# Performance work log

Hardware: AMD Instinct MI355X
Metric: run time of the kernel (lower is better)

Reference implementation:

```python
import jax, jax.numpy as jnp
import numpy as np

N_EMBED = 1024
HEAD_SIZE = 64
BLOCK_SIZE = 2048

def setup_inputs() -> dict:
    key = jax.random.key(0)
    kx, kq, kk, kv = jax.random.split(key, 4)
    scale = N_EMBED ** -0.5
    x = jax.random.normal(kx, (8, 2048, N_EMBED), dtype=jnp.float32)
    # nn.Linear weights stored as [out, in]; we keep [in, out] for x @ W
    Wq = jax.random.normal(kq, (N_EMBED, HEAD_SIZE), dtype=jnp.float32) * scale
    Wk = jax.random.normal(kk, (N_EMBED, HEAD_SIZE), dtype=jnp.float32) * scale
    Wv = jax.random.normal(kv, (N_EMBED, HEAD_SIZE), dtype=jnp.float32) * scale
    return {"x": x, "Wq": Wq, "Wk": Wk, "Wv": Wv}

def reference(x, Wq, Wk, Wv):
    B, T, C = x.shape
    q = x @ Wq  # [B,T,H]
    k = x @ Wk
    v = x @ Wv
    # NOTE: original scales by C**-0.5 (n_embed), not head_size**-0.5
    wei = jnp.einsum('bth,bsh->bts', q, k) * (C ** -0.5)  # [B,T,T]
    causal = jnp.tril(jnp.ones((T, T), dtype=bool))
    wei = jnp.where(causal, wei, -jnp.inf)
    wei = jax.nn.softmax(wei, axis=-1)
    out = jnp.einsum('bts,bsh->bth', wei, v)  # [B,T,H]
    return out
```

## Files before the change

### kernel.cpp

```cpp
#include <hip/hip_runtime.h>

#define B_ 8
#define T_ 2048
#define C_ 1024
#define H_ 64

typedef __attribute__((ext_vector_type(8))) short short8;
typedef __attribute__((ext_vector_type(4))) float floatx4;
typedef __attribute__((ext_vector_type(4))) int intx4;

static __device__ __forceinline__ unsigned short f2bf(float f) {
  unsigned int u = __builtin_bit_cast(unsigned int, f);
  u += 0x7FFFu + ((u >> 16) & 1u);
  return (unsigned short)(u >> 16);
}
static __device__ __forceinline__ float bf2f(unsigned short u) {
  return __builtin_bit_cast(float, ((unsigned int)u) << 16);
}
static __device__ __forceinline__ unsigned int fbits(float f) {
  return __builtin_bit_cast(unsigned int, f);
}

typedef const __attribute__((address_space(1))) unsigned int* gp1_t;
typedef __attribute__((address_space(3))) unsigned int* lp3_t;
static __device__ __forceinline__ void gl_lds16(const void* g, void* l) {
  __builtin_amdgcn_global_load_lds((gp1_t)g, (lp3_t)l, 16, 0, 0);
}

__global__ __launch_bounds__(256) void conv_w(const float* __restrict__ wq,
    const float* __restrict__ wk, const float* __restrict__ wv,
    unsigned short* __restrict__ wf) {
  int c = blockIdx.x * 256 + threadIdx.x;
  int lane = c & 63;
  int t = c >> 6;
  int ng = t % 12;
  int kk = t / 12;
  int k0 = kk * 32 + (lane >> 4) * 8;
  int n = ng * 16 + (lane & 15);
  const float* src;
  int col;
  float scale = 1.0f;
  if (n < 64)       { src = wq; col = n;       scale = 0.03125f * 1.44269504088896340736f; }
  else if (n < 128) { src = wk; col = n - 64;  }
  else              { src = wv; col = n - 128; }
  unsigned short o[8];
#pragma unroll
  for (int j = 0; j < 8; ++j) o[j] = f2bf(src[(size_t)(k0 + j) * H_ + col] * scale);
  *(uint4*)&wf[(size_t)c * 8] = *(const uint4*)o;
}

__global__ __launch_bounds__(256, 4) void qkv_proj(
    const float* __restrict__ x, const unsigned short* __restrict__ wf,
    unsigned short* __restrict__ qo, unsigned short* __restrict__ kf,
    unsigned short* __restrict__ vf) {
  __shared__ float XL[2][4096];
  int tid = threadIdx.x;
  int wave = tid >> 6, lane = tid & 63;
  int lane4 = lane & 15, quad = lane >> 4;
  int m0 = blockIdx.x * 32;
  int ph0 = blockIdx.x & 7;

  auto stage_ph = [&](int phr, int buf) {
#pragma unroll
    for (int j = 0; j < 4; ++j) {
      int c = (wave * 4 + j) * 64 + lane;
      int r = c >> 5, pc = c & 31;
      int cl = (pc & ~7) | ((pc ^ (r & 7)) & 7);
      gl_lds16(&x[(size_t)(m0 + r) * C_ + phr * 128 + cl * 4], &XL[buf][c * 4]);
    }
  };

  floatx4 acc[2][3];
#pragma unroll
  for (int mt = 0; mt < 2; ++mt)
#pragma unroll
    for (int nt = 0; nt < 3; ++nt) acc[mt][nt] = (floatx4)0.0f;

  stage_ph(ph0, 0);
  __syncthreads();

  for (int ph = 0; ph < 8; ++ph) {
    int buf = ph & 1;
    if (ph < 7) stage_ph((ph + 1 + ph0) & 7, buf ^ 1);
    int phr = (ph + ph0) & 7;
#pragma unroll
    for (int sl = 0; sl < 4; ++sl) {
      int s = phr * 4 + sl;
      short8 b[3];
#pragma unroll
      for (int nt = 0; nt < 3; ++nt)
        b[nt] = *(const short8*)&wf[(size_t)(s * 12 + wave * 3 + nt) * 512 + lane * 8];
      short8 a[2];
#pragma unroll
      for (int mt = 0; mt < 2; ++mt) {
        int r = mt * 16 + lane4;
        int c0 = sl * 8 + quad * 2;
        int pc0 = (c0 & ~7) | ((c0 ^ (r & 7)) & 7);
        int pc1 = ((c0 + 1) & ~7) | (((c0 + 1) ^ (r & 7)) & 7);
        float4 f0 = *(const float4*)&XL[buf][r * 128 + pc0 * 4];
        float4 f1 = *(const float4*)&XL[buf][r * 128 + pc1 * 4];
        intx4 pk;
        pk[0] = (int)__builtin_amdgcn_perm(fbits(f0.y), fbits(f0.x), 0x07060302u);
        pk[1] = (int)__builtin_amdgcn_perm(fbits(f0.w), fbits(f0.z), 0x07060302u);
        pk[2] = (int)__builtin_amdgcn_perm(fbits(f1.y), fbits(f1.x), 0x07060302u);
        pk[3] = (int)__builtin_amdgcn_perm(fbits(f1.w), fbits(f1.z), 0x07060302u);
        a[mt] = __builtin_bit_cast(short8, pk);
      }
#pragma unroll
      for (int mt = 0; mt < 2; ++mt)
#pragma unroll
        for (int nt = 0; nt < 3; ++nt)
          acc[mt][nt] = __builtin_amdgcn_mfma_f32_16x16x32_bf16(a[mt], b[nt], acc[mt][nt], 0, 0, 0);
    }
    __syncthreads();
  }

  unsigned short* VTB = (unsigned short*)&XL[0][0];
  unsigned short* KB  = VTB + 5120;
#pragma unroll
  for (int mt = 0; mt < 2; ++mt)
#pragma unroll
    for (int nt = 0; nt < 3; ++nt) {
      int n = wave * 48 + nt * 16 + lane4;
#pragma unroll
      for (int rr = 0; rr < 4; ++rr) {
        unsigned short val = f2bf(acc[mt][nt][rr]);
        int lrow = mt * 16 + quad * 4 + rr;
        if (n < 64)       qo[(size_t)(m0 + lrow) * H_ + n] = val;
        else if (n < 128) KB[lrow * 72 + (n - 64)] = val;
        else              VTB[(n - 128) * 40 + lrow] = val;
      }
    }
  __syncthreads();
  {
    int bb = m0 >> 11, t0 = m0 & 2047;
    int st = t0 >> 6, off = t0 & 63;
    int ks = tid >> 7, ctl = (tid >> 6) & 1, ln = tid & 63;
    int ct = (off >> 4) + ctl;
    int tl = ctl * 16 + (ln & 15);
    int h0 = ks * 32 + (ln >> 4) * 8;
    uint4 kd = *(const uint4*)&KB[tl * 72 + h0];
    *(uint4*)&kf[((size_t)((bb * 32 + st) * 2 + ks) * 4 + ct) * 512 + ln * 8] = kd;
    int nt = tid >> 6, l4 = tid & 15, qs = (tid >> 4) & 3;
    int ksv = off >> 5;
    uint2 vlo = *(const uint2*)&VTB[(nt * 16 + l4) * 40 + qs * 4];
    uint2 vhi = *(const uint2*)&VTB[(nt * 16 + l4) * 40 + 16 + qs * 4];
    uint4 vd = make_uint4(vlo.x, vlo.y, vhi.x, vhi.y);
    *(uint4*)&vf[((size_t)((bb * 32 + st) * 2 + ksv) * 4 + nt) * 512 + (tid & 63) * 8] = vd;
  }
}

__global__ __launch_bounds__(512, 4) void attn(
    const unsigned short* __restrict__ qi, const unsigned short* __restrict__ Kf,
    const unsigned short* __restrict__ Vf, unsigned short* __restrict__ Op,
    float* __restrict__ lsum) {
  __shared__ unsigned short KV[3][8192];

  int tid = threadIdx.x;
  int wave = tid >> 6, lane = tid & 63;
  int lane4 = lane & 15, quad = lane >> 4;
  int split = blockIdx.z;
  int qt = (split < 2) ? (15 - (int)blockIdx.x) : (int)blockIdx.x;
  int b = blockIdx.y;
  int qb = qt * 128;
  int base = b * T_;

  int ntile = 2 * qt + 2;
  int sBeg = (split * ntile) >> 2;
  int sEnd = ((split + 1) * ntile) >> 2;
  int last = sEnd - 1;

  short8 aq[2];
#pragma unroll
  for (int ks = 0; ks < 2; ++ks)
    aq[ks] = *(const short8*)&qi[(size_t)(base + qb + wave * 16 + lane4) * H_ + ks * 32 + quad * 8];

  float lsumv = 0.0f;
  floatx4 o[4];
#pragma unroll
  for (int nt = 0; nt < 4; ++nt) o[nt] = (floatx4)0.0f;

  auto stage = [&](int st, int bf) {
    size_t tb = (size_t)(b * 32 + st) * 4096;
    gl_lds16(&Kf[tb + (size_t)tid * 8], &KV[bf][tid * 8]);
    gl_lds16(&Vf[tb + (size_t)tid * 8], &KV[bf][4096 + tid * 8]);
  };

  if (sBeg < sEnd) {
    stage(sBeg, 0);
    {
      int s1 = sBeg + 1 <= last ? sBeg + 1 : last;
      stage(s1, 1);
    }

    for (int it = 0; it < sEnd - sBeg; ++it) {
      int st = sBeg + it;
      int buf = it % 3;

      asm volatile("s_waitcnt vmcnt(2)" ::: "memory");
      __builtin_amdgcn_sched_barrier(0);
      __builtin_amdgcn_s_barrier();

      {
        int s2 = st + 2 <= last ? st + 2 : last;
        stage(s2, (it + 2) % 3);
      }

      floatx4 sacc[4];
#pragma unroll
      for (int ct = 0; ct < 4; ++ct) sacc[ct] = (floatx4)0.0f;
      __builtin_amdgcn_s_setprio(1);
#pragma unroll
      for (int ks = 0; ks < 2; ++ks)
#pragma unroll
        for (int ct = 0; ct < 4; ++ct) {
          short8 bk = *(const short8*)&KV[buf][(ks * 4 + ct) * 512 + lane * 8];
          sacc[ct] = __builtin_amdgcn_mfma_f32_16x16x32_bf16(bk, aq[ks], sacc[ct], 0, 0, 0);
        }
      __builtin_amdgcn_s_setprio(0);

      if (st >= 2 * qt) {
        int qrow = qb + wave * 16 + lane4;
#pragma unroll
        for (int ct = 0; ct < 4; ++ct)
#pragma unroll
          for (int r = 0; r < 4; ++r) {
            int scol = st * 64 + ct * 16 + quad * 4 + r;
            if (scol > qrow) sacc[ct][r] = -3.0e38f;
          }
      }

      unsigned int pk[4][2];
#pragma unroll
      for (int ct = 0; ct < 4; ++ct) {
        float p0 = exp2f(sacc[ct][0] - 8.0f);
        float p1 = exp2f(sacc[ct][1] - 8.0f);
        float p2 = exp2f(sacc[ct][2] - 8.0f);
        float p3 = exp2f(sacc[ct][3] - 8.0f);
        lsumv += (p0 + p1) + (p2 + p3);
        pk[ct][0] = __builtin_amdgcn_perm(fbits(p1), fbits(p0), 0x07060302u);
        pk[ct][1] = __builtin_amdgcn_perm(fbits(p3), fbits(p2), 0x07060302u);
      }

      __builtin_amdgcn_s_setprio(1);
#pragma unroll
      for (int ks = 0; ks < 2; ++ks) {
        intx4 pai;
        pai[0] = (int)pk[2 * ks][0];
        pai[1] = (int)pk[2 * ks][1];
        pai[2] = (int)pk[2 * ks + 1][0];
        pai[3] = (int)pk[2 * ks + 1][1];
        short8 pa = __builtin_bit_cast(short8, pai);
#pragma unroll
        for (int nt = 0; nt < 4; ++nt) {
          short8 bv = *(const short8*)&KV[buf][4096 + (ks * 4 + nt) * 512 + lane * 8];
          o[nt] = __builtin_amdgcn_mfma_f32_16x16x32_bf16(pa, bv, o[nt], 0, 0, 0);
        }
      }
      __builtin_amdgcn_s_setprio(0);
    }
  }

  lsumv += __shfl_xor(lsumv, 16);
  lsumv += __shfl_xor(lsumv, 32);

  size_t pbase = (((size_t)split * 8 + b) * 16 + qt) * 128;
#pragma unroll
  for (int r = 0; r < 4; ++r) {
    int row = wave * 16 + quad * 4 + r;
#pragma unroll
    for (int nt = 0; nt < 4; ++nt)
      Op[(pbase + row) * 64 + nt * 16 + lane4] = f2bf(o[nt][r]);
  }
  if (quad == 0) lsum[pbase + wave * 16 + lane4] = lsumv;
}

__global__ __launch_bounds__(256) void merge_splits(
    const unsigned short* __restrict__ Op, const float* __restrict__ lsum,
    float* __restrict__ out) {
  int idx = blockIdx.x * 256 + threadIdx.x;
  int row = idx >> 4;
  int h4 = (idx & 15) * 4;
  int b = row >> 11, t = row & 2047;
  int qt = t >> 7, r = t & 127;
  float O0 = 0.f, O1 = 0.f, O2 = 0.f, O3 = 0.f, l = 0.f;
#pragma unroll
  for (int s = 0; s < 4; ++s) {
    size_t p = (((size_t)s * 8 + b) * 16 + qt) * 128 + r;
    l += lsum[p];
    ushort4 ov = *(const ushort4*)&Op[p * 64 + h4];
    O0 += bf2f(ov.x); O1 += bf2f(ov.y); O2 += bf2f(ov.z); O3 += bf2f(ov.w);
  }
  float inv = 1.0f / l;
  float4 res = make_float4(O0 * inv, O1 * inv, O2 * inv, O3 * inv);
  *(float4*)&out[(size_t)row * H_ + h4] = res;
}

extern "C" void kernel_launch(void* const* d_in, const int* in_sizes, int n_in,
                              void* d_out, int out_size, void* d_ws, size_t ws_size,
                              hipStream_t stream) {
  const float* x  = (const float*)d_in[0];
  const float* wq = (const float*)d_in[1];
  const float* wk = (const float*)d_in[2];
  const float* wv = (const float*)d_in[3];
  float* out = (float*)d_out;

  char* ws = (char*)d_ws;
  unsigned short* wf = (unsigned short*)ws;
  unsigned short* qb = (unsigned short*)(ws + 393216);
  unsigned short* kf = (unsigned short*)(ws + 2490368);
  unsigned short* vf = (unsigned short*)(ws + 4587520);
  unsigned short* Op = (unsigned short*)(ws + 6684672);
  float*          ls = (float*)(ws + 15073280);

  conv_w<<<96, 256, 0, stream>>>(wq, wk, wv, wf);
  qkv_proj<<<512, 256, 0, stream>>>(x, wf, qb, kf, vf);
  attn<<<dim3(16, 8, 4), 512, 0, stream>>>(qb, kf, vf, Op, ls);
  merge_splits<<<1024, 256, 0, stream>>>(Op, ls, out);
}
```

Before: 121.6 us.

## Process two 16-row query subtiles per wave in attention kernel

The attention block shrinks from 8 to 4 waves, and each wave now handles 32 query rows (two 16-row subtiles) instead of 16. Each K and V fragment read from LDS then feeds two MFMAs, halving LDS traffic per FLOP. Staging loads double per thread and the wait count is adjusted to match. The trade-off is higher register pressure and fewer waves per block to hide latency, with launch bounds set to 256 threads and 2 blocks per CU.

```diff
diff --git a/kernel.cpp b/kernel.cpp
--- a/kernel.cpp
+++ b/kernel.cpp
@@ -150,7 +150,7 @@
   }
 }
 
-__global__ __launch_bounds__(512, 4) void attn(
+__global__ __launch_bounds__(256, 2) void attn(
     const unsigned short* __restrict__ qi, const unsigned short* __restrict__ Kf,
     const unsigned short* __restrict__ Vf, unsigned short* __restrict__ Op,
     float* __restrict__ lsum) {
@@ -170,20 +170,26 @@
   int sEnd = ((split + 1) * ntile) >> 2;
   int last = sEnd - 1;
 
-  short8 aq[2];
-#pragma unroll
-  for (int ks = 0; ks < 2; ++ks)
-    aq[ks] = *(const short8*)&qi[(size_t)(base + qb + wave * 16 + lane4) * H_ + ks * 32 + quad * 8];
-
-  float lsumv = 0.0f;
-  floatx4 o[4];
-#pragma unroll
-  for (int nt = 0; nt < 4; ++nt) o[nt] = (floatx4)0.0f;
+  short8 aq[2][2];
+#pragma unroll
+  for (int sp = 0; sp < 2; ++sp)
+#pragma unroll
+    for (int ks = 0; ks < 2; ++ks)
+      aq[sp][ks] = *(const short8*)&qi[(size_t)(base + qb + wave * 32 + sp * 16 + lane4) * H_ + ks * 32 + quad * 8];
+
+  float lsumv0 = 0.0f, lsumv1 = 0.0f;
+  floatx4 o[2][4];
+#pragma unroll
+  for (int sp = 0; sp < 2; ++sp)
+#pragma unroll
+    for (int nt = 0; nt < 4; ++nt) o[sp][nt] = (floatx4)0.0f;
 
   auto stage = [&](int st, int bf) {
     size_t tb = (size_t)(b * 32 + st) * 4096;
     gl_lds16(&Kf[tb + (size_t)tid * 8], &KV[bf][tid * 8]);
+    gl_lds16(&Kf[tb + (size_t)(tid + 256) * 8], &KV[bf][(tid + 256) * 8]);
     gl_lds16(&Vf[tb + (size_t)tid * 8], &KV[bf][4096 + tid * 8]);
+    gl_lds16(&Vf[tb + (size_t)(tid + 256) * 8], &KV[bf][4096 + (tid + 256) * 8]);
   };
 
   if (sBeg < sEnd) {
@@ -197,7 +203,7 @@
       int st = sBeg + it;
       int buf = it % 3;
 
-      asm volatile("s_waitcnt vmcnt(2)" ::: "memory");
+      asm volatile("s_waitcnt vmcnt(4)" ::: "memory");
       __builtin_amdgcn_sched_barrier(0);
       __builtin_amdgcn_s_barrier();
 
@@ -206,73 +212,95 @@
         stage(s2, (it + 2) % 3);
       }
 
-      floatx4 sacc[4];
-#pragma unroll
-      for (int ct = 0; ct < 4; ++ct) sacc[ct] = (floatx4)0.0f;
+      floatx4 sacc[2][4];
+#pragma unroll
+      for (int sp = 0; sp < 2; ++sp)
+#pragma unroll
+        for (int ct = 0; ct < 4; ++ct) sacc[sp][ct] = (floatx4)0.0f;
       __builtin_amdgcn_s_setprio(1);
 #pragma unroll
       for (int ks = 0; ks < 2; ++ks)
 #pragma unroll
         for (int ct = 0; ct < 4; ++ct) {
           short8 bk = *(const short8*)&KV[buf][(ks * 4 + ct) * 512 + lane * 8];
-          sacc[ct] = __builtin_amdgcn_mfma_f32_16x16x32_bf16(bk, aq[ks], sacc[ct], 0, 0, 0);
+          sacc[0][ct] = __builtin_amdgcn_mfma_f32_16x16x32_bf16(bk, aq[0][ks], sacc[0][ct], 0, 0, 0);
+          sacc[1][ct] = __builtin_amdgcn_mfma_f32_16x16x32_bf16(bk, aq[1][ks], sacc[1][ct], 0, 0, 0);
         }
       __builtin_amdgcn_s_setprio(0);
 
       if (st >= 2 * qt) {
-        int qrow = qb + wave * 16 + lane4;
-#pragma unroll
-        for (int ct = 0; ct < 4; ++ct)
-#pragma unroll
-          for (int r = 0; r < 4; ++r) {
-            int scol = st * 64 + ct * 16 + quad * 4 + r;
-            if (scol > qrow) sacc[ct][r] = -3.0e38f;
-          }
-      }
-
-      unsigned int pk[4][2];
-#pragma unroll
-      for (int ct = 0; ct < 4; ++ct) {
-        float p0 = exp2f(sacc[ct][0] - 8.0f);
-        float p1 = exp2f(sacc[ct][1] - 8.0f);
-        float p2 = exp2f(sacc[ct][2] - 8.0f);
-        float p3 = exp2f(sacc[ct][3] - 8.0f);
-        lsumv += (p0 + p1) + (p2 + p3);
-        pk[ct][0] = __builtin_amdgcn_perm(fbits(p1), fbits(p0), 0x07060302u);
-        pk[ct][1] = __builtin_amdgcn_perm(fbits(p3), fbits(p2), 0x07060302u);
-      }
+#pragma unroll
+        for (int sp = 0; sp < 2; ++sp) {
+          int qrow = qb + wave * 32 + sp * 16 + lane4;
+#pragma unroll
+          for (int ct = 0; ct < 4; ++ct)
+#pragma unroll
+            for (int r = 0; r < 4; ++r) {
+              int scol = st * 64 + ct * 16 + quad * 4 + r;
+              if (scol > qrow) sacc[sp][ct][r] = -3.0e38f;
+            }
+        }
+      }
+
+      unsigned int pk[2][4][2];
+#pragma unroll
+      for (int sp = 0; sp < 2; ++sp)
+#pragma unroll
+        for (int ct = 0; ct < 4; ++ct) {
+          float p0 = exp2f(sacc[sp][ct][0] - 8.0f);
+          float p1 = exp2f(sacc[sp][ct][1] - 8.0f);
+          float p2 = exp2f(sacc[sp][ct][2] - 8.0f);
+          float p3 = exp2f(sacc[sp][ct][3] - 8.0f);
+          if (sp == 0) lsumv0 += (p0 + p1) + (p2 + p3);
+          else         lsumv1 += (p0 + p1) + (p2 + p3);
+          pk[sp][ct][0] = __builtin_amdgcn_perm(fbits(p1), fbits(p0), 0x07060302u);
+          pk[sp][ct][1] = __builtin_amdgcn_perm(fbits(p3), fbits(p2), 0x07060302u);
+        }
 
       __builtin_amdgcn_s_setprio(1);
 #pragma unroll
       for (int ks = 0; ks < 2; ++ks) {
-        intx4 pai;
-        pai[0] = (int)pk[2 * ks][0];
-        pai[1] = (int)pk[2 * ks][1];
-        pai[2] = (int)pk[2 * ks + 1][0];
-        pai[3] = (int)pk[2 * ks + 1][1];
-        short8 pa = __builtin_bit_cast(short8, pai);
+        intx4 pai0, pai1;
+        pai0[0] = (int)pk[0][2 * ks][0];
+        pai0[1] = (int)pk[0][2 * ks][1];
+        pai0[2] = (int)pk[0][2 * ks + 1][0];
+        pai0[3] = (int)pk[0][2 * ks + 1][1];
+        pai1[0] = (int)pk[1][2 * ks][0];
+        pai1[1] = (int)pk[1][2 * ks][1];
+        pai1[2] = (int)pk[1][2 * ks + 1][0];
+        pai1[3] = (int)pk[1][2 * ks + 1][1];
+        short8 pa0 = __builtin_bit_cast(short8, pai0);
+        short8 pa1 = __builtin_bit_cast(short8, pai1);
 #pragma unroll
         for (int nt = 0; nt < 4; ++nt) {
           short8 bv = *(const short8*)&KV[buf][4096 + (ks * 4 + nt) * 512 + lane * 8];
-          o[nt] = __builtin_amdgcn_mfma_f32_16x16x32_bf16(pa, bv, o[nt], 0, 0, 0);
+          o[0][nt] = __builtin_amdgcn_mfma_f32_16x16x32_bf16(pa0, bv, o[0][nt], 0, 0, 0);
+          o[1][nt] = __builtin_amdgcn_mfma_f32_16x16x32_bf16(pa1, bv, o[1][nt], 0, 0, 0);
         }
       }
       __builtin_amdgcn_s_setprio(0);
     }
   }
 
-  lsumv += __shfl_xor(lsumv, 16);
-  lsumv += __shfl_xor(lsumv, 32);
+  lsumv0 += __shfl_xor(lsumv0, 16);
+  lsumv0 += __shfl_xor(lsumv0, 32);
+  lsumv1 += __shfl_xor(lsumv1, 16);
+  lsumv1 += __shfl_xor(lsumv1, 32);
 
   size_t pbase = (((size_t)split * 8 + b) * 16 + qt) * 128;
 #pragma unroll
-  for (int r = 0; r < 4; ++r) {
-    int row = wave * 16 + quad * 4 + r;
-#pragma unroll
-    for (int nt = 0; nt < 4; ++nt)
-      Op[(pbase + row) * 64 + nt * 16 + lane4] = f2bf(o[nt][r]);
-  }
-  if (quad == 0) lsum[pbase + wave * 16 + lane4] = lsumv;
+  for (int sp = 0; sp < 2; ++sp)
+#pragma unroll
+    for (int r = 0; r < 4; ++r) {
+      int row = wave * 32 + sp * 16 + quad * 4 + r;
+#pragma unroll
+      for (int nt = 0; nt < 4; ++nt)
+        Op[(pbase + row) * 64 + nt * 16 + lane4] = f2bf(o[sp][nt][r]);
+    }
+  if (quad == 0) {
+    lsum[pbase + wave * 32 + lane4] = lsumv0;
+    lsum[pbase + wave * 32 + 16 + lane4] = lsumv1;
+  }
 }
 
 __global__ __launch_bounds__(256) void merge_splits(
@@ -315,6 +343,6 @@
 
   conv_w<<<96, 256, 0, stream>>>(wq, wk, wv, wf);
   qkv_proj<<<512, 256, 0, stream>>>(x, wf, qb, kf, vf);
-  attn<<<dim3(16, 8, 4), 512, 0, stream>>>(qb, kf, vf, Op, ls);
+  attn<<<dim3(16, 8, 4), 256, 0, stream>>>(qb, kf, vf, Op, ls);
   merge_splits<<<1024, 256, 0, stream>>>(Op, ls, out);
 }
```

New measurement: 123.2 us. Within noise of the previous version (+1.3%).
